# Kernel tuning notes

Measured on AMD Instinct MI355X. Metric: run time of the kernel, lower is better.

The kernel has to match this reference:

```python
import jax, jax.numpy as jnp
import numpy as np


def setup_inputs() -> dict:
    key = jax.random.key(0)
    ks = jax.random.split(key, 5)
    B, C, H, W = 8, 256, 64, 64
    Cq = C // 8
    x = jax.random.normal(ks[0], (B, C, H, W), dtype=jnp.float32)
    # kaiming-uniform-ish scale for 1x1 convs (fan_in = C)
    s = float(np.sqrt(1.0 / C))
    Wq = jax.random.normal(ks[1], (Cq, C), dtype=jnp.float32) * s
    Wk = jax.random.normal(ks[2], (Cq, C), dtype=jnp.float32) * s
    Wv = jax.random.normal(ks[3], (C, C), dtype=jnp.float32) * s
    bq = jnp.zeros((Cq,), dtype=jnp.float32)
    bk = jnp.zeros((Cq,), dtype=jnp.float32)
    bv = jnp.zeros((C,), dtype=jnp.float32)
    gamma = jax.random.uniform(ks[4], (1,), dtype=jnp.float32)
    return {"x": x, "Wq": Wq, "bq": bq, "Wk": Wk, "bk": bk, "Wv": Wv, "bv": bv, "gamma": gamma}


def reference(x, Wq, bq, Wk, bk, Wv, bv, gamma):
    B, C, H, W = x.shape
    flat = x.reshape(B, C, H * W)                       # [B, C, N]
    # 1x1 conv == channel matmul
    q = jnp.einsum('oc,bcn->bon', Wq, flat) + bq[None, :, None]   # [B, C/8, N]
    k = jnp.einsum('oc,bcn->bon', Wk, flat) + bk[None, :, None]   # [B, C/8, N]
    v = jnp.einsum('oc,bcn->bon', Wv, flat) + bv[None, :, None]   # [B, C,   N]
    # query permuted to [B, N, C/8]; query_key = bmm -> [B, N, N]
    qk = jnp.einsum('bcn,bcm->bnm', q, k)               # [B, N, N]
    attn = jax.nn.softmax(qk, axis=1)                   # softmax over dim=1 (non-standard)
    out = jnp.einsum('bcn,bnm->bcm', v, attn)           # [B, C, N]
    out = out.reshape(B, C, H, W)
    return gamma[0] * out + x
```

## Files before the change

kernel.cpp:

```cpp
#include <hip/hip_runtime.h>
#include <hip/hip_bf16.h>

#define B_   8
#define C_   256
#define CQ_  32
#define N_   4096
#define OC_  320

typedef __bf16 bf16;
typedef __attribute__((ext_vector_type(8))) __bf16 bf16x8;
typedef __attribute__((ext_vector_type(4))) __bf16 bf16x4;
typedef __attribute__((ext_vector_type(4))) float f32x4;

#define LOG2E 1.4426950408889634f

#define QT_OFF ((size_t)0)
#define KT_OFF ((size_t)B_*N_*CQ_)
#define VB_OFF ((size_t)2*B_*N_*CQ_)
#define WB_OFF (VB_OFF + (size_t)B_*C_*N_)
#define XT_OFF (WB_OFF + (size_t)OC_*C_)
#define WS_END_BF16 (XT_OFF + (size_t)B_*N_*C_)
#define BIAS_BYTE (WS_END_BF16*2)
#define WS_BYTES (BIAS_BYTE + OC_*4)

__device__ inline float exp2_hw(float x) {
  float r;
  asm("v_exp_f32 %0, %1" : "=v"(r) : "v"(x));
  return r;
}

__global__ __launch_bounds__(256) void prep_w(
    const float* __restrict__ Wq, const float* __restrict__ bq,
    const float* __restrict__ Wk, const float* __restrict__ bk,
    const float* __restrict__ Wv, const float* __restrict__ bv,
    bf16* __restrict__ ws)
{
  const int idx = blockIdx.x*256 + threadIdx.x;
  const int o = idx >> 8, c = idx & 255;
  const float v = (o < 32) ? Wq[o*C_ + c]
                : (o < 64) ? Wk[(o-32)*C_ + c]
                           : Wv[(o-64)*C_ + c];
  ws[WB_OFF + idx] = (bf16)v;
  if (idx < OC_) {
    const float bb = (idx < 32) ? bq[idx] : (idx < 64) ? bk[idx-32] : bv[idx-64];
    ((float*)((char*)ws + BIAS_BYTE))[idx] = bb;
  }
}

__global__ __launch_bounds__(256) void prep_x(
    const float* __restrict__ x, bf16* __restrict__ ws)
{
  const int b  = blockIdx.z;
  const int n  = blockIdx.x*64 + (threadIdx.x & 63);
  const int c0 = blockIdx.y*32 + (threadIdx.x >> 6)*8;
  const float* xp = x + ((size_t)b*C_ + c0)*N_ + n;
  bf16x8 pk;
  #pragma unroll
  for (int j = 0; j < 8; ++j) pk[j] = (bf16)xp[(size_t)j*N_];
  *(bf16x8*)(ws + XT_OFF + ((size_t)b*N_ + n)*C_ + c0) = pk;
}

__global__ __launch_bounds__(256) void qkv_mfma(
    const bf16* __restrict__ wsc, bf16* __restrict__ ws)
{
  const int b   = blockIdx.y;
  const int n0  = blockIdx.x * 64;
  const int tid = threadIdx.x, lane = tid & 63;
  const int w   = __builtin_amdgcn_readfirstlane(tid >> 6);
  const int lm  = lane & 15, g = lane >> 4;
  const int obase = w*80;

  const bf16*  Wb   = wsc + WB_OFF;
  const bf16*  xT   = wsc + XT_OFF + (size_t)b*N_*C_;
  const float* bias = (const float*)((const char*)wsc + BIAS_BYTE);

  f32x4 acc[5][4];
  #pragma unroll
  for (int ot = 0; ot < 5; ++ot)
    #pragma unroll
    for (int nt = 0; nt < 4; ++nt)
      acc[ot][nt] = (f32x4){0.f, 0.f, 0.f, 0.f};

  for (int kk = 0; kk < 8; ++kk) {
    bf16x8 wa[5], xf[4];
    #pragma unroll
    for (int ot = 0; ot < 5; ++ot)
      wa[ot] = *(const bf16x8*)(Wb + (size_t)(obase + ot*16 + lm)*C_ + kk*32 + g*8);
    #pragma unroll
    for (int nt = 0; nt < 4; ++nt)
      xf[nt] = *(const bf16x8*)(xT + (size_t)(n0 + nt*16 + lm)*C_ + kk*32 + g*8);
    #pragma unroll
    for (int ot = 0; ot < 5; ++ot)
      #pragma unroll
      for (int nt = 0; nt < 4; ++nt)
        acc[ot][nt] = __builtin_amdgcn_mfma_f32_16x16x32_bf16(
                        wa[ot], xf[nt], acc[ot][nt], 0, 0, 0);
  }

  float bv4[5][4];
  #pragma unroll
  for (int ot = 0; ot < 5; ++ot)
    #pragma unroll
    for (int r = 0; r < 4; ++r)
      bv4[ot][r] = bias[obase + ot*16 + g*4 + r];

  bf16* qT = ws + QT_OFF + (size_t)b*N_*CQ_;
  bf16* kT = ws + KT_OFF + (size_t)b*N_*CQ_;
  bf16* vb = ws + VB_OFF + (size_t)b*C_*N_;

  #pragma unroll
  for (int ot = 0; ot < 5; ++ot) {
    const int O = obase + ot*16;
    #pragma unroll
    for (int nt = 0; nt < 4; ++nt) {
      const int n = n0 + nt*16 + lm;
      if (O < 32) {
        bf16x4 pk;
        #pragma unroll
        for (int r = 0; r < 4; ++r)
          pk[r] = (bf16)((acc[ot][nt][r] + bv4[ot][r]) * LOG2E);
        *(bf16x4*)(qT + (size_t)n*CQ_ + O + g*4) = pk;
      } else if (O < 64) {
        bf16x4 pk;
        #pragma unroll
        for (int r = 0; r < 4; ++r) pk[r] = (bf16)(acc[ot][nt][r] + bv4[ot][r]);
        *(bf16x4*)(kT + (size_t)n*CQ_ + (O - 32) + g*4) = pk;
      } else {
        #pragma unroll
        for (int r = 0; r < 4; ++r)
          vb[(size_t)(O - 64 + g*4 + r)*N_ + n] = (bf16)(acc[ot][nt][r] + bv4[ot][r]);
      }
    }
  }
}

__global__ __launch_bounds__(512, 4) void attn_kernel(
    const bf16* __restrict__ ws, const float* __restrict__ x,
    const float* __restrict__ gamma, float* __restrict__ out)
{
  const int bid  = blockIdx.x;
  const int b    = bid & 7;
  const int m0   = (bid >> 3) << 6;
  const int tid  = threadIdx.x;
  const int lane = tid & 63;
  const int w    = __builtin_amdgcn_readfirstlane(tid >> 6);
  const int lm   = lane & 15;
  const int g    = lane >> 4;

  const bf16* qT = ws + QT_OFF + (size_t)b*N_*CQ_;
  const bf16* kT = ws + KT_OFF + (size_t)b*N_*CQ_;
  const bf16* vb = ws + VB_OFF + (size_t)b*C_*N_;

  __shared__ __align__(16) char Pb[2][64*256];
  __shared__ float red[8][64];
  __shared__ float dsh[64];

  bf16x8 kb[4];
  #pragma unroll
  for (int ms = 0; ms < 4; ++ms)
    kb[ms] = *(const bf16x8*)(kT + (size_t)(m0 + ms*16 + lm)*CQ_ + g*8);

  f32x4 acc[2][4];
  #pragma unroll
  for (int cs = 0; cs < 2; ++cs)
    #pragma unroll
    for (int ms = 0; ms < 4; ++ms)
      acc[cs][ms] = (f32x4){0.f, 0.f, 0.f, 0.f};
  float colsum[4] = {0.f, 0.f, 0.f, 0.f};

  const int c0  = w*32;
  const int swb = w*32 + g*8;
  const f32x4 zero4 = (f32x4){0.f, 0.f, 0.f, 0.f};

  for (int t = 0; t < 32; ++t) {
    const int n0 = t*128;

    bf16x8 vfA[2][2];
    #pragma unroll
    for (int cs = 0; cs < 2; ++cs)
      #pragma unroll
      for (int kc = 0; kc < 2; ++kc)
        vfA[cs][kc] = *(const bf16x8*)(vb + (size_t)(c0 + cs*16 + lm)*N_
                                          + n0 + kc*32 + g*8);
    bf16x8 qf = *(const bf16x8*)(qT + (size_t)(n0 + w*16 + lm)*CQ_ + g*8);

    f32x4 s[4];
    #pragma unroll
    for (int ms = 0; ms < 4; ++ms)
      s[ms] = __builtin_amdgcn_mfma_f32_16x16x32_bf16(qf, kb[ms], zero4, 0, 0, 0);

    char* pbuf = Pb[t & 1];
    #pragma unroll
    for (int ms = 0; ms < 4; ++ms) {
      float p0 = exp2_hw(s[ms][0]);
      float p1 = exp2_hw(s[ms][1]);
      float p2 = exp2_hw(s[ms][2]);
      float p3 = exp2_hw(s[ms][3]);
      colsum[ms] += (p0 + p1) + (p2 + p3);
      bf16x4 pk;
      pk[0] = (bf16)p0; pk[1] = (bf16)p1; pk[2] = (bf16)p2; pk[3] = (bf16)p3;
      const int m = lm + 16*ms;
      *(bf16x4*)(pbuf + m*256 + (swb ^ ((m & 7) << 4))) = pk;
    }
    __syncthreads();

    bf16x8 vfB[2][2];
    #pragma unroll
    for (int cs = 0; cs < 2; ++cs)
      #pragma unroll
      for (int kc = 0; kc < 2; ++kc)
        vfB[cs][kc] = *(const bf16x8*)(vb + (size_t)(c0 + cs*16 + lm)*N_
                                          + n0 + 64 + kc*32 + g*8);

    #pragma unroll
    for (int kc = 0; kc < 4; ++kc)
      #pragma unroll
      for (int ms = 0; ms < 4; ++ms) {
        const int m = lm + 16*ms;
        bf16x8 pf = *(const bf16x8*)(pbuf + m*256
                                     + ((kc*64 + g*16) ^ ((m & 7) << 4)));
        #pragma unroll
        for (int cs = 0; cs < 2; ++cs)
          acc[cs][ms] = __builtin_amdgcn_mfma_f32_16x16x32_bf16(
                          (kc < 2) ? vfA[cs][kc] : vfB[cs][kc-2],
                          pf, acc[cs][ms], 0, 0, 0);
      }
  }

  #pragma unroll
  for (int ms = 0; ms < 4; ++ms) {
    colsum[ms] += __shfl_xor(colsum[ms], 16, 64);
    colsum[ms] += __shfl_xor(colsum[ms], 32, 64);
  }
  if (lane < 16) {
    #pragma unroll
    for (int ms = 0; ms < 4; ++ms) red[w][lm + 16*ms] = colsum[ms];
  }
  __syncthreads();
  if (tid < 64) {
    float sden = 0.f;
    #pragma unroll
    for (int r2 = 0; r2 < 8; ++r2) sden += red[r2][tid];
    dsh[tid] = sden;
  }
  __syncthreads();

  const float gam = gamma[0];
  float inv[4];
  #pragma unroll
  for (int ms = 0; ms < 4; ++ms) inv[ms] = gam / dsh[lm + 16*ms];

  #pragma unroll
  for (int cs = 0; cs < 2; ++cs)
    #pragma unroll
    for (int ms = 0; ms < 4; ++ms)
      #pragma unroll
      for (int r = 0; r < 4; ++r) {
        const int c = c0 + cs*16 + g*4 + r;
        const int m = m0 + 16*ms + lm;
        const size_t idx = ((size_t)b*C_ + c)*N_ + m;
        out[idx] = acc[cs][ms][r] * inv[ms] + x[idx];
      }
}

extern "C" void kernel_launch(void* const* d_in, const int* in_sizes, int n_in,
                              void* d_out, int out_size, void* d_ws, size_t ws_size,
                              hipStream_t stream) {
  const float* x     = (const float*)d_in[0];
  const float* Wq    = (const float*)d_in[1];
  const float* bq    = (const float*)d_in[2];
  const float* Wk    = (const float*)d_in[3];
  const float* bk    = (const float*)d_in[4];
  const float* Wv    = (const float*)d_in[5];
  const float* bv    = (const float*)d_in[6];
  const float* gamma = (const float*)d_in[7];
  float* out = (float*)d_out;
  bf16* ws   = (bf16*)d_ws;

  if (ws_size < WS_BYTES) return;

  prep_w<<<320, 256, 0, stream>>>(Wq, bq, Wk, bk, Wv, bv, ws);
  prep_x<<<dim3(64, 8, 8), 256, 0, stream>>>(x, ws);
  qkv_mfma<<<dim3(64, 8), 256, 0, stream>>>(ws, ws);
  attn_kernel<<<512, 512, 0, stream>>>(ws, x, gamma, out);
}
```

Before: 176.2 us.

## Software-pipeline Q and V loads one tile ahead in attention loop

The main attention loop is unrolled by two with ping-pong register sets, so the next tile's Q fragment and first-half V fragments are loaded during the current tile's PV MFMAs. Pointer arithmetic is precomputed into base pointers. The inline-asm exp2 is replaced with the compiler builtin, which lets the compiler schedule it. The aim is to hide global load latency behind compute, at the cost of higher register pressure under the 512x4 launch bounds.

```diff
diff --git a/kernel.cpp b/kernel.cpp
--- a/kernel.cpp
+++ b/kernel.cpp
@@ -24,9 +24,7 @@
 #define WS_BYTES (BIAS_BYTE + OC_*4)
 
 __device__ inline float exp2_hw(float x) {
-  float r;
-  asm("v_exp_f32 %0, %1" : "=v"(r) : "v"(x));
-  return r;
+  return __builtin_amdgcn_exp2f(x);
 }
 
 __global__ __launch_bounds__(256) void prep_w(
@@ -134,6 +132,58 @@
   }
 }
 
+#define TILE_BODY(T, QF, VF, QN, VN, PBUF)                                    \
+  {                                                                           \
+    f32x4 s[4];                                                               \
+    _Pragma("unroll")                                                         \
+    for (int ms = 0; ms < 4; ++ms)                                            \
+      s[ms] = __builtin_amdgcn_mfma_f32_16x16x32_bf16(QF, kb[ms], zero4, 0, 0, 0); \
+    _Pragma("unroll")                                                         \
+    for (int ms = 0; ms < 4; ++ms) {                                          \
+      float p0 = exp2_hw(s[ms][0]);                                           \
+      float p1 = exp2_hw(s[ms][1]);                                           \
+      float p2 = exp2_hw(s[ms][2]);                                           \
+      float p3 = exp2_hw(s[ms][3]);                                           \
+      colsum[ms] += (p0 + p1) + (p2 + p3);                                    \
+      bf16x4 pk;                                                              \
+      pk[0] = (bf16)p0; pk[1] = (bf16)p1; pk[2] = (bf16)p2; pk[3] = (bf16)p3; \
+      const int m = lm + 16*ms;                                               \
+      *(bf16x4*)((PBUF) + m*256 + (swb ^ ((m & 7) << 4))) = pk;               \
+    }                                                                         \
+    __syncthreads();                                                          \
+                        \
+    bf16x8 vfC[2][2];                                                         \
+    _Pragma("unroll")                                                         \
+    for (int cs = 0; cs < 2; ++cs)                                            \
+      _Pragma("unroll")                                                       \
+      for (int kc = 0; kc < 2; ++kc)                                          \
+        vfC[cs][kc] = *(const bf16x8*)(vp0 + (size_t)cs*16*N_                 \
+                                       + (size_t)(T)*128 + 64 + kc*32);       \
+                   \
+    {                                                                         \
+      const size_t pn = (size_t)(((T) + 1 < 32) ? (T) + 1 : 31) * 128;        \
+      QN = *(const bf16x8*)(qp + pn*CQ_);                                     \
+      _Pragma("unroll")                                                       \
+      for (int cs = 0; cs < 2; ++cs)                                          \
+        _Pragma("unroll")                                                     \
+        for (int kc = 0; kc < 2; ++kc)                                        \
+          VN[cs][kc] = *(const bf16x8*)(vp0 + (size_t)cs*16*N_ + pn + kc*32); \
+    }                                                                         \
+    _Pragma("unroll")                                                         \
+    for (int kc = 0; kc < 4; ++kc)                                            \
+      _Pragma("unroll")                                                       \
+      for (int ms = 0; ms < 4; ++ms) {                                        \
+        const int m = lm + 16*ms;                                             \
+        bf16x8 pf = *(const bf16x8*)((PBUF) + m*256                           \
+                                     + ((kc*64 + g*16) ^ ((m & 7) << 4)));    \
+        _Pragma("unroll")                                                     \
+        for (int cs = 0; cs < 2; ++cs)                                        \
+          acc[cs][ms] = __builtin_amdgcn_mfma_f32_16x16x32_bf16(              \
+                          (kc < 2) ? VF[cs][kc] : vfC[cs][kc-2],              \
+                          pf, acc[cs][ms], 0, 0, 0);                          \
+      }                                                                       \
+  }
+
 __global__ __launch_bounds__(512, 4) void attn_kernel(
     const bf16* __restrict__ ws, const float* __restrict__ x,
     const float* __restrict__ gamma, float* __restrict__ out)
@@ -172,59 +222,23 @@
   const int swb = w*32 + g*8;
   const f32x4 zero4 = (f32x4){0.f, 0.f, 0.f, 0.f};
 
-  for (int t = 0; t < 32; ++t) {
-    const int n0 = t*128;
-
-    bf16x8 vfA[2][2];
-    #pragma unroll
-    for (int cs = 0; cs < 2; ++cs)
-      #pragma unroll
-      for (int kc = 0; kc < 2; ++kc)
-        vfA[cs][kc] = *(const bf16x8*)(vb + (size_t)(c0 + cs*16 + lm)*N_
-                                          + n0 + kc*32 + g*8);
-    bf16x8 qf = *(const bf16x8*)(qT + (size_t)(n0 + w*16 + lm)*CQ_ + g*8);
-
-    f32x4 s[4];
-    #pragma unroll
-    for (int ms = 0; ms < 4; ++ms)
-      s[ms] = __builtin_amdgcn_mfma_f32_16x16x32_bf16(qf, kb[ms], zero4, 0, 0, 0);
-
-    char* pbuf = Pb[t & 1];
-    #pragma unroll
-    for (int ms = 0; ms < 4; ++ms) {
-      float p0 = exp2_hw(s[ms][0]);
-      float p1 = exp2_hw(s[ms][1]);
-      float p2 = exp2_hw(s[ms][2]);
-      float p3 = exp2_hw(s[ms][3]);
-      colsum[ms] += (p0 + p1) + (p2 + p3);
-      bf16x4 pk;
-      pk[0] = (bf16)p0; pk[1] = (bf16)p1; pk[2] = (bf16)p2; pk[3] = (bf16)p3;
-      const int m = lm + 16*ms;
-      *(bf16x4*)(pbuf + m*256 + (swb ^ ((m & 7) << 4))) = pk;
-    }
-    __syncthreads();
-
-    bf16x8 vfB[2][2];
-    #pragma unroll
-    for (int cs = 0; cs < 2; ++cs)
-      #pragma unroll
-      for (int kc = 0; kc < 2; ++kc)
-        vfB[cs][kc] = *(const bf16x8*)(vb + (size_t)(c0 + cs*16 + lm)*N_
-                                          + n0 + 64 + kc*32 + g*8);
-
-    #pragma unroll
-    for (int kc = 0; kc < 4; ++kc)
-      #pragma unroll
-      for (int ms = 0; ms < 4; ++ms) {
-        const int m = lm + 16*ms;
-        bf16x8 pf = *(const bf16x8*)(pbuf + m*256
-                                     + ((kc*64 + g*16) ^ ((m & 7) << 4)));
-        #pragma unroll
-        for (int cs = 0; cs < 2; ++cs)
-          acc[cs][ms] = __builtin_amdgcn_mfma_f32_16x16x32_bf16(
-                          (kc < 2) ? vfA[cs][kc] : vfB[cs][kc-2],
-                          pf, acc[cs][ms], 0, 0, 0);
-      }
+  const bf16* qp  = qT + (size_t)(w*16 + lm)*CQ_ + g*8;
+  const bf16* vp0 = vb + (size_t)(c0 + lm)*N_ + g*8;
+
+  bf16x8 qfA = *(const bf16x8*)(qp);
+  bf16x8 vfA[2][2];
+  #pragma unroll
+  for (int cs = 0; cs < 2; ++cs)
+    #pragma unroll
+    for (int kc = 0; kc < 2; ++kc)
+      vfA[cs][kc] = *(const bf16x8*)(vp0 + (size_t)cs*16*N_ + kc*32);
+  bf16x8 qfB;
+  bf16x8 vfB[2][2];
+
+  for (int tt = 0; tt < 16; ++tt) {
+    const int t0 = 2*tt;
+    TILE_BODY(t0,     qfA, vfA, qfB, vfB, Pb[0]);
+    TILE_BODY(t0 + 1, qfB, vfB, qfA, vfA, Pb[1]);
   }
 
   #pragma unroll
```

Result: slower. 204.0 us (+15.8%).

## Process two key tiles per barrier in attention loop with quad LDS buffers

Applied to the files above, without the earlier changes.

The attention main loop now handles two 128-wide n tiles per iteration, writing both probability tiles to LDS before a single barrier. This halves the number of __syncthreads and gives the scheduler more independent MFMA, exp and global-load work to interleave. The LDS P buffer grows from 2 to 4 slots (64KB), which may lower occupancy below the 4 blocks per CU launch bound, and register pressure also rises. The inline-asm v_exp_f32 is replaced by the compiler builtin so the compiler can schedule it.

```diff
diff --git a/kernel.cpp b/kernel.cpp
--- a/kernel.cpp
+++ b/kernel.cpp
@@ -24,9 +24,7 @@
 #define WS_BYTES (BIAS_BYTE + OC_*4)
 
 __device__ inline float exp2_hw(float x) {
-  float r;
-  asm("v_exp_f32 %0, %1" : "=v"(r) : "v"(x));
-  return r;
+  return __builtin_amdgcn_exp2f(x);
 }
 
 __global__ __launch_bounds__(256) void prep_w(
@@ -151,7 +149,7 @@
   const bf16* kT = ws + KT_OFF + (size_t)b*N_*CQ_;
   const bf16* vb = ws + VB_OFF + (size_t)b*C_*N_;
 
-  __shared__ __align__(16) char Pb[2][64*256];
+  __shared__ __align__(16) char Pb[4][64*256];
   __shared__ float red[8][64];
   __shared__ float dsh[64];
 
@@ -172,58 +170,110 @@
   const int swb = w*32 + g*8;
   const f32x4 zero4 = (f32x4){0.f, 0.f, 0.f, 0.f};
 
-  for (int t = 0; t < 32; ++t) {
-    const int n0 = t*128;
-
-    bf16x8 vfA[2][2];
+  const bf16* qp  = qT + (size_t)(w*16 + lm)*CQ_ + g*8;
+  const bf16* vp0 = vb + (size_t)(c0 + lm)*N_ + g*8;
+
+  for (int p = 0; p < 16; ++p) {
+    const size_t n0 = (size_t)p * 256;
+    const size_t n1 = n0 + 128;
+    char* pb0 = Pb[(p & 1)*2 + 0];
+    char* pb1 = Pb[(p & 1)*2 + 1];
+
+    bf16x8 qf0 = *(const bf16x8*)(qp + n0*CQ_);
+    bf16x8 qf1 = *(const bf16x8*)(qp + n1*CQ_);
+    bf16x8 vfA0[2][2], vfA1[2][2];
     #pragma unroll
     for (int cs = 0; cs < 2; ++cs)
       #pragma unroll
-      for (int kc = 0; kc < 2; ++kc)
-        vfA[cs][kc] = *(const bf16x8*)(vb + (size_t)(c0 + cs*16 + lm)*N_
-                                          + n0 + kc*32 + g*8);
-    bf16x8 qf = *(const bf16x8*)(qT + (size_t)(n0 + w*16 + lm)*CQ_ + g*8);
-
-    f32x4 s[4];
-    #pragma unroll
-    for (int ms = 0; ms < 4; ++ms)
-      s[ms] = __builtin_amdgcn_mfma_f32_16x16x32_bf16(qf, kb[ms], zero4, 0, 0, 0);
-
-    char* pbuf = Pb[t & 1];
+      for (int kc = 0; kc < 2; ++kc) {
+        vfA0[cs][kc] = *(const bf16x8*)(vp0 + (size_t)cs*16*N_ + n0 + kc*32);
+        vfA1[cs][kc] = *(const bf16x8*)(vp0 + (size_t)cs*16*N_ + n1 + kc*32);
+      }
+
+    f32x4 s0[4], s1[4];
     #pragma unroll
     for (int ms = 0; ms < 4; ++ms) {
-      float p0 = exp2_hw(s[ms][0]);
-      float p1 = exp2_hw(s[ms][1]);
-      float p2 = exp2_hw(s[ms][2]);
-      float p3 = exp2_hw(s[ms][3]);
-      colsum[ms] += (p0 + p1) + (p2 + p3);
-      bf16x4 pk;
-      pk[0] = (bf16)p0; pk[1] = (bf16)p1; pk[2] = (bf16)p2; pk[3] = (bf16)p3;
+      s0[ms] = __builtin_amdgcn_mfma_f32_16x16x32_bf16(qf0, kb[ms], zero4, 0, 0, 0);
+      s1[ms] = __builtin_amdgcn_mfma_f32_16x16x32_bf16(qf1, kb[ms], zero4, 0, 0, 0);
+    }
+
+    #pragma unroll
+    for (int ms = 0; ms < 4; ++ms) {
       const int m = lm + 16*ms;
-      *(bf16x4*)(pbuf + m*256 + (swb ^ ((m & 7) << 4))) = pk;
+      const int wo = m*256 + (swb ^ ((m & 7) << 4));
+      float a0 = exp2_hw(s0[ms][0]), a1 = exp2_hw(s0[ms][1]);
+      float a2 = exp2_hw(s0[ms][2]), a3 = exp2_hw(s0[ms][3]);
+      float b0 = exp2_hw(s1[ms][0]), b1 = exp2_hw(s1[ms][1]);
+      float b2 = exp2_hw(s1[ms][2]), b3 = exp2_hw(s1[ms][3]);
+      colsum[ms] += ((a0 + a1) + (a2 + a3)) + ((b0 + b1) + (b2 + b3));
+      bf16x4 pk0, pk1;
+      pk0[0] = (bf16)a0; pk0[1] = (bf16)a1; pk0[2] = (bf16)a2; pk0[3] = (bf16)a3;
+      pk1[0] = (bf16)b0; pk1[1] = (bf16)b1; pk1[2] = (bf16)b2; pk1[3] = (bf16)b3;
+      *(bf16x4*)(pb0 + wo) = pk0;
+      *(bf16x4*)(pb1 + wo) = pk1;
     }
     __syncthreads();
 
-    bf16x8 vfB[2][2];
+    bf16x8 vfB0[2][2];
     #pragma unroll
     for (int cs = 0; cs < 2; ++cs)
       #pragma unroll
       for (int kc = 0; kc < 2; ++kc)
-        vfB[cs][kc] = *(const bf16x8*)(vb + (size_t)(c0 + cs*16 + lm)*N_
-                                          + n0 + 64 + kc*32 + g*8);
-
-    #pragma unroll
-    for (int kc = 0; kc < 4; ++kc)
+        vfB0[cs][kc] = *(const bf16x8*)(vp0 + (size_t)cs*16*N_ + n0 + 64 + kc*32);
+
+    #pragma unroll
+    for (int kc = 0; kc < 2; ++kc)
       #pragma unroll
       for (int ms = 0; ms < 4; ++ms) {
         const int m = lm + 16*ms;
-        bf16x8 pf = *(const bf16x8*)(pbuf + m*256
-                                     + ((kc*64 + g*16) ^ ((m & 7) << 4)));
+        bf16x8 pf = *(const bf16x8*)(pb0 + m*256 + ((kc*64 + g*16) ^ ((m & 7) << 4)));
         #pragma unroll
         for (int cs = 0; cs < 2; ++cs)
           acc[cs][ms] = __builtin_amdgcn_mfma_f32_16x16x32_bf16(
-                          (kc < 2) ? vfA[cs][kc] : vfB[cs][kc-2],
-                          pf, acc[cs][ms], 0, 0, 0);
+                          vfA0[cs][kc], pf, acc[cs][ms], 0, 0, 0);
+      }
+
+    bf16x8 vfB1[2][2];
+    #pragma unroll
+    for (int cs = 0; cs < 2; ++cs)
+      #pragma unroll
+      for (int kc = 0; kc < 2; ++kc)
+        vfB1[cs][kc] = *(const bf16x8*)(vp0 + (size_t)cs*16*N_ + n1 + 64 + kc*32);
+
+    #pragma unroll
+    for (int kc = 0; kc < 2; ++kc)
+      #pragma unroll
+      for (int ms = 0; ms < 4; ++ms) {
+        const int m = lm + 16*ms;
+        bf16x8 pf = *(const bf16x8*)(pb0 + m*256 + (((kc+2)*64 + g*16) ^ ((m & 7) << 4)));
+        #pragma unroll
+        for (int cs = 0; cs < 2; ++cs)
+          acc[cs][ms] = __builtin_amdgcn_mfma_f32_16x16x32_bf16(
+                          vfB0[cs][kc], pf, acc[cs][ms], 0, 0, 0);
+      }
+
+    #pragma unroll
+    for (int kc = 0; kc < 2; ++kc)
+      #pragma unroll
+      for (int ms = 0; ms < 4; ++ms) {
+        const int m = lm + 16*ms;
+        bf16x8 pf = *(const bf16x8*)(pb1 + m*256 + ((kc*64 + g*16) ^ ((m & 7) << 4)));
+        #pragma unroll
+        for (int cs = 0; cs < 2; ++cs)
+          acc[cs][ms] = __builtin_amdgcn_mfma_f32_16x16x32_bf16(
+                          vfA1[cs][kc], pf, acc[cs][ms], 0, 0, 0);
+      }
+
+    #pragma unroll
+    for (int kc = 0; kc < 2; ++kc)
+      #pragma unroll
+      for (int ms = 0; ms < 4; ++ms) {
+        const int m = lm + 16*ms;
+        bf16x8 pf = *(const bf16x8*)(pb1 + m*256 + (((kc+2)*64 + g*16) ^ ((m & 7) << 4)));
+        #pragma unroll
+        for (int cs = 0; cs < 2; ++cs)
+          acc[cs][ms] = __builtin_amdgcn_mfma_f32_16x16x32_bf16(
+                          vfB1[cs][kc], pf, acc[cs][ms], 0, 0, 0);
       }
   }
 
```

Measured after the change: 202.0 us. 14.6% more time.

## Split attention output channels across two blocks and raise occupancy

Applied to the files above, without the earlier changes.

Each attention block now computes only 128 of the 256 output channels, doubling the grid to 1024 blocks and halving accumulator registers per wave. Launch bounds request 6 waves-per-EU instead of 4, and the LDS swizzle gains an extra bit to spread bank conflicts. The trade-off is that the QK^T scores and exp must be recomputed twice per column tile, duplicating softmax work and K/Q loads.

```diff
diff --git a/kernel.cpp b/kernel.cpp
--- a/kernel.cpp
+++ b/kernel.cpp
@@ -24,9 +24,11 @@
 #define WS_BYTES (BIAS_BYTE + OC_*4)
 
 __device__ inline float exp2_hw(float x) {
-  float r;
-  asm("v_exp_f32 %0, %1" : "=v"(r) : "v"(x));
-  return r;
+  return __builtin_amdgcn_exp2f(x);
+}
+
+__device__ inline int swz(int m) {
+  return ((m & 7) << 4) ^ (((m >> 3) & 1) << 7);
 }
 
 __global__ __launch_bounds__(256) void prep_w(
@@ -134,13 +136,14 @@
   }
 }
 
-__global__ __launch_bounds__(512, 4) void attn_kernel(
+__global__ __launch_bounds__(512, 6) void attn_kernel(
     const bf16* __restrict__ ws, const float* __restrict__ x,
     const float* __restrict__ gamma, float* __restrict__ out)
 {
   const int bid  = blockIdx.x;
   const int b    = bid & 7;
-  const int m0   = (bid >> 3) << 6;
+  const int m0   = ((bid >> 3) & 63) << 6;
+  const int c0b  = (bid >> 9) << 7;
   const int tid  = threadIdx.x;
   const int lane = tid & 63;
   const int w    = __builtin_amdgcn_readfirstlane(tid >> 6);
@@ -160,36 +163,34 @@
   for (int ms = 0; ms < 4; ++ms)
     kb[ms] = *(const bf16x8*)(kT + (size_t)(m0 + ms*16 + lm)*CQ_ + g*8);
 
-  f32x4 acc[2][4];
-  #pragma unroll
-  for (int cs = 0; cs < 2; ++cs)
-    #pragma unroll
-    for (int ms = 0; ms < 4; ++ms)
-      acc[cs][ms] = (f32x4){0.f, 0.f, 0.f, 0.f};
+  f32x4 acc[4];
+  #pragma unroll
+  for (int ms = 0; ms < 4; ++ms)
+    acc[ms] = (f32x4){0.f, 0.f, 0.f, 0.f};
   float colsum[4] = {0.f, 0.f, 0.f, 0.f};
 
-  const int c0  = w*32;
+  const int cb  = c0b + w*16;
   const int swb = w*32 + g*8;
   const f32x4 zero4 = (f32x4){0.f, 0.f, 0.f, 0.f};
 
+  const bf16* qp  = qT + (size_t)(w*16 + lm)*CQ_ + g*8;
+  const bf16* vp  = vb + (size_t)(cb + lm)*N_ + g*8;
+
   for (int t = 0; t < 32; ++t) {
-    const int n0 = t*128;
-
-    bf16x8 vfA[2][2];
-    #pragma unroll
-    for (int cs = 0; cs < 2; ++cs)
-      #pragma unroll
-      for (int kc = 0; kc < 2; ++kc)
-        vfA[cs][kc] = *(const bf16x8*)(vb + (size_t)(c0 + cs*16 + lm)*N_
-                                          + n0 + kc*32 + g*8);
-    bf16x8 qf = *(const bf16x8*)(qT + (size_t)(n0 + w*16 + lm)*CQ_ + g*8);
+    const size_t n0 = (size_t)t * 128;
+    char* pbuf = Pb[t & 1];
+
+    bf16x8 qf = *(const bf16x8*)(qp + n0*CQ_);
+    bf16x8 vfA[2];
+    #pragma unroll
+    for (int kc = 0; kc < 2; ++kc)
+      vfA[kc] = *(const bf16x8*)(vp + n0 + kc*32);
 
     f32x4 s[4];
     #pragma unroll
     for (int ms = 0; ms < 4; ++ms)
       s[ms] = __builtin_amdgcn_mfma_f32_16x16x32_bf16(qf, kb[ms], zero4, 0, 0, 0);
 
-    char* pbuf = Pb[t & 1];
     #pragma unroll
     for (int ms = 0; ms < 4; ++ms) {
       float p0 = exp2_hw(s[ms][0]);
@@ -200,17 +201,14 @@
       bf16x4 pk;
       pk[0] = (bf16)p0; pk[1] = (bf16)p1; pk[2] = (bf16)p2; pk[3] = (bf16)p3;
       const int m = lm + 16*ms;
-      *(bf16x4*)(pbuf + m*256 + (swb ^ ((m & 7) << 4))) = pk;
+      *(bf16x4*)(pbuf + m*256 + (swb ^ swz(m))) = pk;
     }
     __syncthreads();
 
-    bf16x8 vfB[2][2];
-    #pragma unroll
-    for (int cs = 0; cs < 2; ++cs)
-      #pragma unroll
-      for (int kc = 0; kc < 2; ++kc)
-        vfB[cs][kc] = *(const bf16x8*)(vb + (size_t)(c0 + cs*16 + lm)*N_
-                                          + n0 + 64 + kc*32 + g*8);
+    bf16x8 vfB[2];
+    #pragma unroll
+    for (int kc = 0; kc < 2; ++kc)
+      vfB[kc] = *(const bf16x8*)(vp + n0 + 64 + kc*32);
 
     #pragma unroll
     for (int kc = 0; kc < 4; ++kc)
@@ -218,12 +216,9 @@
       for (int ms = 0; ms < 4; ++ms) {
         const int m = lm + 16*ms;
         bf16x8 pf = *(const bf16x8*)(pbuf + m*256
-                                     + ((kc*64 + g*16) ^ ((m & 7) << 4)));
-        #pragma unroll
-        for (int cs = 0; cs < 2; ++cs)
-          acc[cs][ms] = __builtin_amdgcn_mfma_f32_16x16x32_bf16(
-                          (kc < 2) ? vfA[cs][kc] : vfB[cs][kc-2],
-                          pf, acc[cs][ms], 0, 0, 0);
+                                     + ((kc*64 + g*16) ^ swz(m)));
+        acc[ms] = __builtin_amdgcn_mfma_f32_16x16x32_bf16(
+                    (kc < 2) ? vfA[kc] : vfB[kc-2], pf, acc[ms], 0, 0, 0);
       }
   }
 
@@ -251,16 +246,14 @@
   for (int ms = 0; ms < 4; ++ms) inv[ms] = gam / dsh[lm + 16*ms];
 
   #pragma unroll
-  for (int cs = 0; cs < 2; ++cs)
-    #pragma unroll
-    for (int ms = 0; ms < 4; ++ms)
-      #pragma unroll
-      for (int r = 0; r < 4; ++r) {
-        const int c = c0 + cs*16 + g*4 + r;
-        const int m = m0 + 16*ms + lm;
-        const size_t idx = ((size_t)b*C_ + c)*N_ + m;
-        out[idx] = acc[cs][ms][r] * inv[ms] + x[idx];
-      }
+  for (int ms = 0; ms < 4; ++ms)
+    #pragma unroll
+    for (int r = 0; r < 4; ++r) {
+      const int c = cb + g*4 + r;
+      const int m = m0 + 16*ms + lm;
+      const size_t idx = ((size_t)b*C_ + c)*N_ + m;
+      out[idx] = acc[ms][r] * inv[ms] + x[idx];
+    }
 }
 
 extern "C" void kernel_launch(void* const* d_in, const int* in_sizes, int n_in,
@@ -282,5 +275,5 @@
   prep_w<<<320, 256, 0, stream>>>(Wq, bq, Wk, bk, Wv, bv, ws);
   prep_x<<<dim3(64, 8, 8), 256, 0, stream>>>(x, ws);
   qkv_mfma<<<dim3(64, 8), 256, 0, stream>>>(ws, ws);
-  attn_kernel<<<512, 512, 0, stream>>>(ws, x, gamma, out);
-}
+  attn_kernel<<<1024, 512, 0, stream>>>(ws, x, gamma, out);
+}
```

Measured after the change: 208.3 us. 1.18x slower.
